# Optimization experiments

Hardware: AMD Instinct MI355X
Metric: run time of the kernel (lower is better)

Reference implementation:

```python
import jax, jax.numpy as jnp
import numpy as np

B, N_Z, N_E, D = 16, 2048, 2048, 512

def setup_inputs() -> dict:
    key = jax.random.key(0)
    kz, ke, km = jax.random.split(key, 3)
    z = jax.random.normal(kz, (B, N_Z, D), dtype=jnp.float32)
    e = jax.random.normal(ke, (B, N_E, D), dtype=jnp.float32)
    M = jax.random.normal(km, (D, D), dtype=jnp.float32)  # init: normal(0, 1)
    return {"z": z, "e": e, "M": M}

def reference(z, e, M):
    # a = z @ M @ e^T : [B, Nz, Ne]
    zM = jnp.einsum('bnd,de->bne', z, M)
    a = jnp.einsum('bnd,bmd->bnm', zM, e)
    a = jax.nn.sigmoid(a)
    # softmax over dim=1 (the Nz axis), as in the torch code
    A = jax.nn.softmax(a, axis=1)
    # out = A @ e : [B, Nz, D]
    return jnp.einsum('bnm,bmd->bnd', A, e)
```

## Files before the change

### kernel.cpp

```cpp
#include <hip/hip_runtime.h>
#include <hip/hip_bf16.h>
#include <stdint.h>

#define BB 16
#define NZ 2048
#define NE 2048
#define DD 512

typedef unsigned short u16;
typedef __attribute__((ext_vector_type(8))) _Float16 f16x8;
typedef __attribute__((ext_vector_type(4))) float f32x4;

__device__ __forceinline__ u16 f2h(float f) {
  _Float16 h = (_Float16)f;
  return __builtin_bit_cast(u16, h);
}

__device__ __forceinline__ float h2f(u16 h) {
  return (float)__builtin_bit_cast(_Float16, h);
}

__device__ __forceinline__ void gload_lds16(const void* g, void* l) {
  auto gp = (const __attribute__((address_space(1))) uint32_t*)g;
  auto lp = (__attribute__((address_space(3))) uint32_t*)l;
  __builtin_amdgcn_global_load_lds(gp, lp, 16, 0, 0);
}

#define FENCE() asm volatile("" ::: "memory")
#define BARRIER() do { FENCE(); __builtin_amdgcn_s_barrier(); FENCE(); } while (0)
#define WAIT_VM(n) asm volatile("s_waitcnt vmcnt(" #n ")" ::: "memory")

__global__ void k_cvt(const float* __restrict__ in, u16* __restrict__ out, int n4) {
  int i = blockIdx.x * blockDim.x + threadIdx.x;
  int stride = gridDim.x * blockDim.x;
  for (; i < n4; i += stride) {
    float4 v = ((const float4*)in)[i];
    ushort4 o;
    o.x = f2h(v.x); o.y = f2h(v.y); o.z = f2h(v.z); o.w = f2h(v.w);
    ((ushort4*)out)[i] = o;
  }
}

__global__ void k_mt(const float* __restrict__ M, u16* __restrict__ Mt) {
  __shared__ float t[32][33];
  int bx = blockIdx.x * 32;
  int by = blockIdx.y * 32;
  for (int r = 0; r < 32; r += 8)
    t[threadIdx.y + r][threadIdx.x] = M[(size_t)(by + threadIdx.y + r) * DD + bx + threadIdx.x];
  __syncthreads();
  for (int r = 0; r < 32; r += 8)
    Mt[(size_t)(bx + threadIdx.y + r) * DD + by + threadIdx.x] = f2h(t[threadIdx.x][threadIdx.y + r]);
}

__global__ void k_et(const u16* __restrict__ eH, const float* __restrict__ cs,
                     u16* __restrict__ eT) {
  __shared__ float t[32][33];
  int b = blockIdx.z;
  int m0 = blockIdx.y * 32, d0 = blockIdx.x * 32;
  const u16* eb = eH + (size_t)b * NE * DD;
  const float* csb = cs + (size_t)b * NE;
  for (int r = 0; r < 32; r += 8) {
    int m = m0 + threadIdx.y + r;
    t[threadIdx.y + r][threadIdx.x] =
        h2f(eb[(size_t)m * DD + d0 + threadIdx.x]) * (2048.0f / csb[m]);
  }
  __syncthreads();
  u16* eTb = eT + (size_t)b * DD * NE;
  for (int r = 0; r < 32; r += 8) {
    int d = d0 + threadIdx.y + r;
    eTb[(size_t)d * NE + m0 + threadIdx.x] = f2h(t[threadIdx.x][threadIdx.y + r]);
  }
}

template<int EPI, int KDIM>
__global__ __launch_bounds__(512, 2) void k_gemm(
    const u16* __restrict__ A, const u16* __restrict__ Bt, void* __restrict__ Cp,
    int Ndim, long long sAb, long long sBb, long long sCb,
    float* __restrict__ colsum, int csld)
{
  extern __shared__ char lds[];
  constexpr int NT = KDIM / 64;

  const int gx = gridDim.x, gy = gridDim.y;
  const int nwg = gx * gy * gridDim.z;
  const int hid = blockIdx.x + gx * (blockIdx.y + gy * blockIdx.z);
  const int logical = (hid & 7) * (nwg >> 3) + (hid >> 3);
  const int bx = logical % gx;
  const int rem0 = logical / gx;
  const int by = rem0 % gy;
  const int bz = rem0 / gy;

  const int tid = threadIdx.x;
  const int lane = tid & 63;
  const int wid = tid >> 6;
  const int wr = wid >> 2;
  const int wc = wid & 3;

  const int row0 = by * 256;
  const int col0 = bx * 256;

  const u16* Ab = A + (long long)bz * sAb;
  const u16* Bb = Bt + (long long)bz * sBb;

  const u16* srcA[4]; const u16* srcB[4];
#pragma unroll
  for (int c = 0; c < 4; ++c) {
    int idx = c * 512 + tid;
    int ks = idx >> 10, rm = idx & 1023;
    int mf = rm >> 6, q = (rm >> 4) & 3, p = rm & 15;
    int r = mf * 16 + p, c8 = ks * 4 + q;
    srcA[c] = Ab + (long long)(row0 + r) * KDIM + c8 * 8;
    srcB[c] = Bb + (long long)(col0 + r) * KDIM + c8 * 8;
  }

  auto stage = [&](char* dA, char* dB, int k0) {
#pragma unroll
    for (int c = 0; c < 2; ++c) {
      gload_lds16(srcA[c] + k0, dA + (c * 512 + wid * 64) * 16);
      gload_lds16(srcB[c] + k0, dB + (c * 512 + wid * 64) * 16);
    }
#pragma unroll
    for (int c = 2; c < 4; ++c) {
      gload_lds16(srcA[c] + k0, dA + (c * 512 + wid * 64) * 16);
      gload_lds16(srcB[c] + k0, dB + (c * 512 + wid * 64) * 16);
    }
  };

  f32x4 acc[8][4] = {};

  stage(lds, lds + 65536, 0);
  WAIT_VM(4);
  BARRIER();

  for (int t = 0; t < NT; ++t) {
    const int buf = t & 1;
    char* lA = lds + buf * 32768;
    char* lB = lds + 65536 + buf * 32768;
    const bool pf = (t + 1 < NT);

    if (pf) stage(lds + (buf ^ 1) * 32768, lds + 65536 + (buf ^ 1) * 32768,
                  (t + 1) * 64);

    {
      f16x8 af[8], bf[4];
#pragma unroll
      for (int m = 0; m < 8; ++m)
        af[m] = *(const f16x8*)(lA + ((0 * 16 + wr * 8 + m) * 64 + lane) * 16);
#pragma unroll
      for (int n = 0; n < 4; ++n)
        bf[n] = *(const f16x8*)(lB + ((0 * 16 + wc * 4 + n) * 64 + lane) * 16);
#pragma unroll
      for (int m = 0; m < 8; ++m)
#pragma unroll
        for (int n = 0; n < 4; ++n)
          acc[m][n] = __builtin_amdgcn_mfma_f32_16x16x32_f16(af[m], bf[n], acc[m][n], 0, 0, 0);
    }
    if (pf) { WAIT_VM(8); } else { WAIT_VM(0); }
    BARRIER();

    {
      f16x8 af[8], bf[4];
#pragma unroll
      for (int m = 0; m < 8; ++m)
        af[m] = *(const f16x8*)(lA + ((1 * 16 + wr * 8 + m) * 64 + lane) * 16);
#pragma unroll
      for (int n = 0; n < 4; ++n)
        bf[n] = *(const f16x8*)(lB + ((1 * 16 + wc * 4 + n) * 64 + lane) * 16);
#pragma unroll
      for (int m = 0; m < 8; ++m)
#pragma unroll
        for (int n = 0; n < 4; ++n)
          acc[m][n] = __builtin_amdgcn_mfma_f32_16x16x32_f16(af[m], bf[n], acc[m][n], 0, 0, 0);
    }
    if (pf) {
      WAIT_VM(4);
      BARRIER();
    }
  }

  const int rr = (lane >> 4) * 4;
  const int cc = lane & 15;
  if constexpr (EPI == 0) {
    u16* C = (u16*)Cp + (long long)bz * sCb;
#pragma unroll
    for (int m = 0; m < 8; ++m)
#pragma unroll
      for (int n = 0; n < 4; ++n)
#pragma unroll
        for (int j = 0; j < 4; ++j) {
          int row = row0 + wr * 128 + m * 16 + rr + j;
          int col = col0 + wc * 64 + n * 16 + cc;
          C[(long long)row * Ndim + col] = f2h(acc[m][n][j]);
        }
  } else if constexpr (EPI == 1) {
    u16* C = (u16*)Cp + (long long)bz * sCb;
    float csum[4] = {0.f, 0.f, 0.f, 0.f};
#pragma unroll
    for (int m = 0; m < 8; ++m)
#pragma unroll
      for (int n = 0; n < 4; ++n)
#pragma unroll
        for (int j = 0; j < 4; ++j) {
          float x = acc[m][n][j];
          float s = 1.f / (1.f + __expf(-x));
          float v = __expf(s);
          int row = row0 + wr * 128 + m * 16 + rr + j;
          int col = col0 + wc * 64 + n * 16 + cc;
          C[(long long)row * Ndim + col] = f2h(v);
          csum[n] += v;
        }
#pragma unroll
    for (int n = 0; n < 4; ++n) {
      float v = csum[n];
      v += __shfl_xor(v, 16, 64);
      v += __shfl_xor(v, 32, 64);
      if ((lane >> 4) == 0)
        atomicAdd(&colsum[(long long)bz * csld + col0 + wc * 64 + n * 16 + cc], v);
    }
  } else {
    float* C = (float*)Cp + (long long)bz * sCb;
#pragma unroll
    for (int m = 0; m < 8; ++m)
#pragma unroll
      for (int n = 0; n < 4; ++n)
#pragma unroll
        for (int j = 0; j < 4; ++j) {
          int row = row0 + wr * 128 + m * 16 + rr + j;
          int col = col0 + wc * 64 + n * 16 + cc;
          C[(long long)row * Ndim + col] = acc[m][n][j] * (1.0f / 2048.0f);
        }
  }
}

extern "C" void kernel_launch(void* const* d_in, const int* in_sizes, int n_in,
                              void* d_out, int out_size, void* d_ws, size_t ws_size,
                              hipStream_t stream) {
  const float* z = (const float*)d_in[0];
  const float* e = (const float*)d_in[1];
  const float* M = (const float*)d_in[2];
  float* out = (float*)d_out;
  char* ws = (char*)d_ws;

  u16* S    = (u16*)(ws + 0LL);
  u16* zM   = (u16*)(ws + 134217728LL);
  u16* zH   = (u16*)(ws + 167772160LL);
  u16* eH   = (u16*)(ws + 201326592LL);
  u16* Mt   = (u16*)(ws + 234881024LL);
  float* cs = (float*)(ws + 235405312LL);

  (void)hipFuncSetAttribute(reinterpret_cast<const void*>(&k_gemm<0, 512>),
                            hipFuncAttributeMaxDynamicSharedMemorySize, 131072);
  (void)hipFuncSetAttribute(reinterpret_cast<const void*>(&k_gemm<1, 512>),
                            hipFuncAttributeMaxDynamicSharedMemorySize, 131072);
  (void)hipFuncSetAttribute(reinterpret_cast<const void*>(&k_gemm<2, 2048>),
                            hipFuncAttributeMaxDynamicSharedMemorySize, 131072);

  hipMemsetAsync(cs, 0, (size_t)BB * NE * sizeof(float), stream);

  k_cvt<<<4096, 256, 0, stream>>>(z, zH, BB * NZ * DD / 4);
  k_cvt<<<4096, 256, 0, stream>>>(e, eH, BB * NE * DD / 4);
  k_mt<<<dim3(16, 16), dim3(32, 8), 0, stream>>>(M, Mt);

  k_gemm<0, 512><<<dim3(DD / 256, (BB * NZ) / 256, 1), 512, 131072, stream>>>(
      zH, Mt, zM, DD, 0LL, 0LL, 0LL, nullptr, 0);

  k_gemm<1, 512><<<dim3(NE / 256, NZ / 256, BB), 512, 131072, stream>>>(
      zM, eH, S, NE,
      (long long)NZ * DD, (long long)NE * DD, (long long)NZ * NE, cs, NE);

  u16* eT = zH;
  k_et<<<dim3(DD / 32, NE / 32, BB), dim3(32, 8), 0, stream>>>(eH, cs, eT);

  k_gemm<2, 2048><<<dim3(DD / 256, NZ / 256, BB), 512, 131072, stream>>>(
      S, eT, out, DD,
      (long long)NZ * NE, (long long)DD * NE, (long long)NZ * DD, nullptr, 0);
}
```

Measured before the change: 285.7 us.

## Shrink GEMM tiles to 128x128 with 256 threads and stage epilogue stores through LDS

```diff
diff --git a/kernel.cpp b/kernel.cpp
--- a/kernel.cpp
+++ b/kernel.cpp
@@ -73,7 +73,7 @@
 }
 
 template<int EPI, int KDIM>
-__global__ __launch_bounds__(512, 2) void k_gemm(
+__global__ __launch_bounds__(256, 2) void k_gemm(
     const u16* __restrict__ A, const u16* __restrict__ Bt, void* __restrict__ Cp,
     int Ndim, long long sAb, long long sBb, long long sCb,
     float* __restrict__ colsum, int csld)
@@ -93,11 +93,11 @@
   const int tid = threadIdx.x;
   const int lane = tid & 63;
   const int wid = tid >> 6;
-  const int wr = wid >> 2;
-  const int wc = wid & 3;
-
-  const int row0 = by * 256;
-  const int col0 = bx * 256;
+  const int wr = wid >> 1;
+  const int wc = wid & 1;
+
+  const int row0 = by * 128;
+  const int col0 = bx * 128;
 
   const u16* Ab = A + (long long)bz * sAb;
   const u16* Bb = Bt + (long long)bz * sBb;
@@ -105,8 +105,8 @@
   const u16* srcA[4]; const u16* srcB[4];
 #pragma unroll
   for (int c = 0; c < 4; ++c) {
-    int idx = c * 512 + tid;
-    int ks = idx >> 10, rm = idx & 1023;
+    int idx = c * 256 + tid;
+    int ks = idx >> 9, rm = idx & 511;
     int mf = rm >> 6, q = (rm >> 4) & 3, p = rm & 15;
     int r = mf * 16 + p, c8 = ks * 4 + q;
     srcA[c] = Ab + (long long)(row0 + r) * KDIM + c8 * 8;
@@ -115,42 +115,40 @@
 
   auto stage = [&](char* dA, char* dB, int k0) {
 #pragma unroll
-    for (int c = 0; c < 2; ++c) {
-      gload_lds16(srcA[c] + k0, dA + (c * 512 + wid * 64) * 16);
-      gload_lds16(srcB[c] + k0, dB + (c * 512 + wid * 64) * 16);
-    }
-#pragma unroll
-    for (int c = 2; c < 4; ++c) {
-      gload_lds16(srcA[c] + k0, dA + (c * 512 + wid * 64) * 16);
-      gload_lds16(srcB[c] + k0, dB + (c * 512 + wid * 64) * 16);
-    }
+    for (int c = 0; c < 2; ++c) gload_lds16(srcA[c] + k0, dA + (c * 256 + wid * 64) * 16);
+#pragma unroll
+    for (int c = 0; c < 2; ++c) gload_lds16(srcB[c] + k0, dB + (c * 256 + wid * 64) * 16);
+#pragma unroll
+    for (int c = 2; c < 4; ++c) gload_lds16(srcA[c] + k0, dA + (c * 256 + wid * 64) * 16);
+#pragma unroll
+    for (int c = 2; c < 4; ++c) gload_lds16(srcB[c] + k0, dB + (c * 256 + wid * 64) * 16);
   };
 
-  f32x4 acc[8][4] = {};
-
-  stage(lds, lds + 65536, 0);
+  f32x4 acc[4][4] = {};
+
+  stage(lds, lds + 32768, 0);
   WAIT_VM(4);
   BARRIER();
 
   for (int t = 0; t < NT; ++t) {
     const int buf = t & 1;
-    char* lA = lds + buf * 32768;
-    char* lB = lds + 65536 + buf * 32768;
+    char* lA = lds + buf * 16384;
+    char* lB = lds + 32768 + buf * 16384;
     const bool pf = (t + 1 < NT);
 
-    if (pf) stage(lds + (buf ^ 1) * 32768, lds + 65536 + (buf ^ 1) * 32768,
+    if (pf) stage(lds + (buf ^ 1) * 16384, lds + 32768 + (buf ^ 1) * 16384,
                   (t + 1) * 64);
 
     {
-      f16x8 af[8], bf[4];
-#pragma unroll
-      for (int m = 0; m < 8; ++m)
-        af[m] = *(const f16x8*)(lA + ((0 * 16 + wr * 8 + m) * 64 + lane) * 16);
-#pragma unroll
-      for (int n = 0; n < 4; ++n)
-        bf[n] = *(const f16x8*)(lB + ((0 * 16 + wc * 4 + n) * 64 + lane) * 16);
-#pragma unroll
-      for (int m = 0; m < 8; ++m)
+      f16x8 af[4], bf[4];
+#pragma unroll
+      for (int m = 0; m < 4; ++m)
+        af[m] = *(const f16x8*)(lA + ((0 * 8 + wr * 4 + m) * 64 + lane) * 16);
+#pragma unroll
+      for (int n = 0; n < 4; ++n)
+        bf[n] = *(const f16x8*)(lB + ((0 * 8 + wc * 4 + n) * 64 + lane) * 16);
+#pragma unroll
+      for (int m = 0; m < 4; ++m)
 #pragma unroll
         for (int n = 0; n < 4; ++n)
           acc[m][n] = __builtin_amdgcn_mfma_f32_16x16x32_f16(af[m], bf[n], acc[m][n], 0, 0, 0);
@@ -159,15 +157,15 @@
     BARRIER();
 
     {
-      f16x8 af[8], bf[4];
-#pragma unroll
-      for (int m = 0; m < 8; ++m)
-        af[m] = *(const f16x8*)(lA + ((1 * 16 + wr * 8 + m) * 64 + lane) * 16);
-#pragma unroll
-      for (int n = 0; n < 4; ++n)
-        bf[n] = *(const f16x8*)(lB + ((1 * 16 + wc * 4 + n) * 64 + lane) * 16);
-#pragma unroll
-      for (int m = 0; m < 8; ++m)
+      f16x8 af[4], bf[4];
+#pragma unroll
+      for (int m = 0; m < 4; ++m)
+        af[m] = *(const f16x8*)(lA + ((1 * 8 + wr * 4 + m) * 64 + lane) * 16);
+#pragma unroll
+      for (int n = 0; n < 4; ++n)
+        bf[n] = *(const f16x8*)(lB + ((1 * 8 + wc * 4 + n) * 64 + lane) * 16);
+#pragma unroll
+      for (int m = 0; m < 4; ++m)
 #pragma unroll
         for (int n = 0; n < 4; ++n)
           acc[m][n] = __builtin_amdgcn_mfma_f32_16x16x32_f16(af[m], bf[n], acc[m][n], 0, 0, 0);
@@ -178,57 +176,78 @@
     }
   }
 
+  BARRIER();
+
   const int rr = (lane >> 4) * 4;
   const int cc = lane & 15;
-  if constexpr (EPI == 0) {
-    u16* C = (u16*)Cp + (long long)bz * sCb;
-#pragma unroll
-    for (int m = 0; m < 8; ++m)
-#pragma unroll
-      for (int n = 0; n < 4; ++n)
-#pragma unroll
-        for (int j = 0; j < 4; ++j) {
-          int row = row0 + wr * 128 + m * 16 + rr + j;
-          int col = col0 + wc * 64 + n * 16 + cc;
-          C[(long long)row * Ndim + col] = f2h(acc[m][n][j]);
-        }
-  } else if constexpr (EPI == 1) {
-    u16* C = (u16*)Cp + (long long)bz * sCb;
+  const int grow = row0 + wr * 64;
+  const int gcol = col0 + wc * 64;
+
+  if constexpr (EPI == 0 || EPI == 1) {
+    char* wb = lds + wid * 8192;
     float csum[4] = {0.f, 0.f, 0.f, 0.f};
 #pragma unroll
-    for (int m = 0; m < 8; ++m)
+    for (int m = 0; m < 4; ++m)
 #pragma unroll
       for (int n = 0; n < 4; ++n)
 #pragma unroll
         for (int j = 0; j < 4; ++j) {
           float x = acc[m][n][j];
-          float s = 1.f / (1.f + __expf(-x));
-          float v = __expf(s);
-          int row = row0 + wr * 128 + m * 16 + rr + j;
-          int col = col0 + wc * 64 + n * 16 + cc;
-          C[(long long)row * Ndim + col] = f2h(v);
-          csum[n] += v;
+          float v;
+          if constexpr (EPI == 1) {
+            float s = 1.f / (1.f + __expf(-x));
+            v = __expf(s);
+            csum[n] += v;
+          } else {
+            v = x;
+          }
+          int rl = m * 16 + rr + j;
+          int col = n * 16 + cc;
+          int chunk = (col >> 3) ^ (rl & 7);
+          *(u16*)(wb + rl * 128 + chunk * 16 + ((col * 2) & 15)) = f2h(v);
         }
-#pragma unroll
-    for (int n = 0; n < 4; ++n) {
-      float v = csum[n];
-      v += __shfl_xor(v, 16, 64);
-      v += __shfl_xor(v, 32, 64);
-      if ((lane >> 4) == 0)
-        atomicAdd(&colsum[(long long)bz * csld + col0 + wc * 64 + n * 16 + cc], v);
+    if constexpr (EPI == 1) {
+#pragma unroll
+      for (int n = 0; n < 4; ++n) {
+        float v = csum[n];
+        v += __shfl_xor(v, 16, 64);
+        v += __shfl_xor(v, 32, 64);
+        if ((lane >> 4) == 0)
+          atomicAdd(&colsum[(long long)bz * csld + gcol + n * 16 + cc], v);
+      }
+    }
+    __syncthreads();
+    u16* C = (u16*)Cp + (long long)bz * sCb;
+#pragma unroll
+    for (int s = 0; s < 8; ++s) {
+      int rl = (lane >> 3) + s * 8;
+      int chunk = (lane & 7) ^ (rl & 7);
+      f16x8 v = *(const f16x8*)(wb + rl * 128 + chunk * 16);
+      *(f16x8*)(&C[(long long)(grow + rl) * Ndim + gcol + (lane & 7) * 8]) = v;
     }
   } else {
+    char* wb = lds + wid * 16384;
+#pragma unroll
+    for (int m = 0; m < 4; ++m)
+#pragma unroll
+      for (int n = 0; n < 4; ++n)
+#pragma unroll
+        for (int j = 0; j < 4; ++j) {
+          int rl = m * 16 + rr + j;
+          int col = n * 16 + cc;
+          int chunk = (col >> 2) ^ (rl & 15);
+          *(float*)(wb + rl * 256 + chunk * 16 + ((col * 4) & 15)) =
+              acc[m][n][j] * (1.0f / 2048.0f);
+        }
+    __syncthreads();
     float* C = (float*)Cp + (long long)bz * sCb;
 #pragma unroll
-    for (int m = 0; m < 8; ++m)
-#pragma unroll
-      for (int n = 0; n < 4; ++n)
-#pragma unroll
-        for (int j = 0; j < 4; ++j) {
-          int row = row0 + wr * 128 + m * 16 + rr + j;
-          int col = col0 + wc * 64 + n * 16 + cc;
-          C[(long long)row * Ndim + col] = acc[m][n][j] * (1.0f / 2048.0f);
-        }
+    for (int s = 0; s < 16; ++s) {
+      int rl = (lane >> 4) + s * 4;
+      int chunk = (lane & 15) ^ (rl & 15);
+      f32x4 v = *(const f32x4*)(wb + rl * 256 + chunk * 16);
+      *(f32x4*)(&C[(long long)(grow + rl) * Ndim + gcol + (lane & 15) * 4]) = v;
+    }
   }
 }
 
@@ -249,11 +268,11 @@
   float* cs = (float*)(ws + 235405312LL);
 
   (void)hipFuncSetAttribute(reinterpret_cast<const void*>(&k_gemm<0, 512>),
-                            hipFuncAttributeMaxDynamicSharedMemorySize, 131072);
+                            hipFuncAttributeMaxDynamicSharedMemorySize, 65536);
   (void)hipFuncSetAttribute(reinterpret_cast<const void*>(&k_gemm<1, 512>),
-                            hipFuncAttributeMaxDynamicSharedMemorySize, 131072);
+                            hipFuncAttributeMaxDynamicSharedMemorySize, 65536);
   (void)hipFuncSetAttribute(reinterpret_cast<const void*>(&k_gemm<2, 2048>),
-                            hipFuncAttributeMaxDynamicSharedMemorySize, 131072);
+                            hipFuncAttributeMaxDynamicSharedMemorySize, 65536);
 
   hipMemsetAsync(cs, 0, (size_t)BB * NE * sizeof(float), stream);
 
@@ -261,17 +280,17 @@
   k_cvt<<<4096, 256, 0, stream>>>(e, eH, BB * NE * DD / 4);
   k_mt<<<dim3(16, 16), dim3(32, 8), 0, stream>>>(M, Mt);
 
-  k_gemm<0, 512><<<dim3(DD / 256, (BB * NZ) / 256, 1), 512, 131072, stream>>>(
+  k_gemm<0, 512><<<dim3(DD / 128, (BB * NZ) / 128, 1), 256, 65536, stream>>>(
       zH, Mt, zM, DD, 0LL, 0LL, 0LL, nullptr, 0);
 
-  k_gemm<1, 512><<<dim3(NE / 256, NZ / 256, BB), 512, 131072, stream>>>(
+  k_gemm<1, 512><<<dim3(NE / 128, NZ / 128, BB), 256, 65536, stream>>>(
       zM, eH, S, NE,
       (long long)NZ * DD, (long long)NE * DD, (long long)NZ * NE, cs, NE);
 
   u16* eT = zH;
   k_et<<<dim3(DD / 32, NE / 32, BB), dim3(32, 8), 0, stream>>>(eH, cs, eT);
 
-  k_gemm<2, 2048><<<dim3(DD / 256, NZ / 256, BB), 512, 131072, stream>>>(
+  k_gemm<2, 2048><<<dim3(DD / 128, NZ / 128, BB), 256, 65536, stream>>>(
       S, eT, out, DD,
       (long long)NZ * NE, (long long)DD * NE, (long long)NZ * DD, nullptr, 0);
 }
```

Result: slower. 362.1 us (+26.8%).
